# Optimization experiments

Hardware: AMD Instinct MI355X
Metric: run time of the kernel (lower is better)

The kernel has to match this reference:

```python
import jax, jax.numpy as jnp
import numpy as np

N_NODES = 100000
N_EDGES = 1600000
C = 256            # in_channels == out_channels
NUM_BUNDLES = 64
BUNDLE_DIM = 2
NUM_GRAPHS = 128
BN_EPS = 1e-5


def setup_inputs() -> dict:
    key = jax.random.key(0)
    ks = jax.random.split(key, 12)
    x = jax.random.normal(ks[0], (N_NODES, C), dtype=jnp.float32)
    edge_index = jax.random.randint(ks[1], (2, N_EDGES), 0, N_NODES, dtype=jnp.int64)
    batch = jnp.sort(jax.random.randint(ks[2], (N_NODES,), 0, NUM_GRAPHS, dtype=jnp.int64))
    s = 0.05
    # struct_enc MLP: Linear(C, 2*NB) -> GELU -> Linear(2*NB, NB)
    se_w1 = jax.random.normal(ks[3], (C, 2 * NUM_BUNDLES), dtype=jnp.float32) * s
    se_b1 = jnp.zeros((2 * NUM_BUNDLES,), dtype=jnp.float32)
    se_w2 = jax.random.normal(ks[4], (2 * NUM_BUNDLES, NUM_BUNDLES), dtype=jnp.float32) * s
    se_b2 = jnp.zeros((NUM_BUNDLES,), dtype=jnp.float32)
    # LimConv.lin: Linear(C, C)
    lin_w = jax.random.normal(ks[5], (C, C), dtype=jnp.float32) * s
    lin_b = jnp.zeros((C,), dtype=jnp.float32)
    # BatchNorm1d affine params
    bn_gamma = jnp.ones((C,), dtype=jnp.float32)
    bn_beta = jnp.zeros((C,), dtype=jnp.float32)
    return {"x": x, "edge_index": edge_index, "batch": batch,
            "se_w1": se_w1, "se_b1": se_b1, "se_w2": se_w2, "se_b2": se_b2,
            "lin_w": lin_w, "lin_b": lin_b, "bn_gamma": bn_gamma, "bn_beta": bn_beta}


def _lim_layer(x, batch, se_w1, se_b1, se_w2, se_b2, lin_w, lin_b, bn_gamma, bn_beta):
    n = x.shape[0]
    # vector field: [N, NB, 2, fiber]
    vf = x.reshape(n, NUM_BUNDLES, BUNDLE_DIM, -1)
    # struct_enc MLP -> per-bundle angle (tanh-squashed), euler map to SO(2)
    h1 = jax.nn.gelu(x @ se_w1 + se_b1, approximate=False)
    ang = jnp.tanh(h1 @ se_w2 + se_b2)          # [N, NB]
    c, s = jnp.cos(ang), jnp.sin(ang)
    # R[n,b] = [[c,-s],[s,c]]  -> [N, NB, 2, 2]
    rot = jnp.stack([jnp.stack([c, -s], axis=-1),
                     jnp.stack([s, c], axis=-1)], axis=-2)
    # rotate fibers
    vf = jnp.einsum('nbij,nbjf->nbif', rot, vf)
    h = vf.reshape(n, C) @ lin_w + lin_b
    # global mean pool over graphs, then broadcast back to nodes
    sums = jax.ops.segment_sum(h, batch, num_segments=NUM_GRAPHS)
    cnts = jax.ops.segment_sum(jnp.ones((n,), h.dtype), batch, num_segments=NUM_GRAPHS)
    hmean = sums / jnp.maximum(cnts, 1.0)[:, None]
    h = hmean[batch]
    # inverse rotation (R^T)
    vf = h.reshape(n, NUM_BUNDLES, BUNDLE_DIM, -1)
    vf = jnp.einsum('nbji,nbjf->nbif', rot, vf)
    h = vf.reshape(n, C)
    # residual (dim_in == dim_out)
    h = x + h
    # dropout p=0 / eval -> identity. BatchNorm1d with batch statistics.
    mu = jnp.mean(h, axis=0)
    var = jnp.var(h, axis=0)
    h = (h - mu) * jax.lax.rsqrt(var + BN_EPS) * bn_gamma + bn_beta
    return h


def reference(x, edge_index, batch, se_w1, se_b1, se_w2, se_b2, lin_w, lin_b, bn_gamma, bn_beta):
    # edge_index is unused when num_gnn == 0 (struct_enc is an MLP), as in the source.
    del edge_index
    return _lim_layer(x, batch, se_w1, se_b1, se_w2, se_b2, lin_w, lin_b, bn_gamma, bn_beta)
```

## Files before the change

### kernel.cpp

```cpp
#include <hip/hip_runtime.h>
#include <hip/hip_bf16.h>
#include <math.h>

#define N_NODES 100000
#define C 256
#define NB 64
#define H1D 128
#define NG 128
#define GS 257
#define BN_EPS 1e-5f

#define BLKN 64
#define NBLK1 ((N_NODES + BLKN - 1) / BLKN)

#define OFF_GSUMS 0
#define OFF_BNSUM (NG * GS)
#define OFF_BNSQ  (OFF_BNSUM + 256)
#define ZERO_FLOATS (OFF_BNSQ + 256)
#define OFF_HMEAN ZERO_FLOATS
#define OFF_WT1   (OFF_HMEAN + NG * C)
#define OFF_WT2   (OFF_WT1 + 16896)
#define OFF_CSN   (OFF_WT2 + 4352)

#define WT1_LD 264
#define WT2_LD 136
#define XS_LD  272

typedef __attribute__((ext_vector_type(8))) short bf16x8;
typedef __attribute__((ext_vector_type(4))) float f32x4;

struct __align__(8) bf4 { __hip_bfloat16 x, y, z, w; };

__device__ __forceinline__ float bf2f(__hip_bfloat16 h) { return __bfloat162float(h); }

__global__ __launch_bounds__(256)
void k0_prep(const float* __restrict__ W1, const float* __restrict__ W2,
             __hip_bfloat16* __restrict__ Wt1, __hip_bfloat16* __restrict__ Wt2)
{
    const int t0 = threadIdx.x + blockIdx.x * 256;
    const int stride = gridDim.x * 256;
    for (int i = t0; i < 128 * 256; i += stride) {
        int n = i >> 8, k = i & 255;
        Wt1[n * WT1_LD + k] = __float2bfloat16(W1[k * 128 + n]);
    }
    for (int i = t0; i < 64 * 128; i += stride) {
        int n = i >> 7, k = i & 127;
        Wt2[n * WT2_LD + k] = __float2bfloat16(W2[k * 64 + n]);
    }
}

__global__ __launch_bounds__(256, 3)
void k1_angles_rot_pool(const float* __restrict__ x,
                        const int* __restrict__ batch,
                        const __hip_bfloat16* __restrict__ Wt1g,
                        const float* __restrict__ b1,
                        const __hip_bfloat16* __restrict__ Wt2g,
                        const float* __restrict__ b2,
                        float* __restrict__ gsums,
                        __hip_bfloat16* __restrict__ csng)
{
    __shared__ __hip_bfloat16 xs[BLKN][XS_LD];
    __shared__ char sm_u[BLKN * WT2_LD * 2];
    __shared__ int gsh[BLKN];
    auto h1s = (__hip_bfloat16 (*)[WT2_LD])sm_u;
    auto csn = (__hip_bfloat16 (*)[132])sm_u;

    const int t = threadIdx.x;
    const int w = t >> 6;
    const int l = t & 63;
    const int lo = l & 15, quad = l >> 4;
    const int n0 = blockIdx.x * BLKN;
    const int nrem = min(BLKN, N_NODES - n0);

    #pragma unroll
    for (int m = 0; m < 16; ++m) {
        int idx = t + m * 256;
        int r = idx >> 6, c4 = (idx & 63) * 4;
        float4 v;
        if (n0 + r < N_NODES) v = *(const float4*)(x + (size_t)(n0 + r) * C + c4);
        else { v.x = v.y = v.z = v.w = 0.f; }
        bf4 pk;
        pk.x = __float2bfloat16(v.x); pk.y = __float2bfloat16(v.y);
        pk.z = __float2bfloat16(v.z); pk.w = __float2bfloat16(v.w);
        *(bf4*)&xs[r][c4] = pk;
    }
    if (t < BLKN) gsh[t] = batch[min(n0 + t, N_NODES - 1)];
    __syncthreads();

    const short* w1base = (const short*)Wt1g + (w * 32 + lo) * WT1_LD + quad * 8;
    f32x4 acc1[4][2];
    #pragma unroll
    for (int mt = 0; mt < 4; ++mt) { acc1[mt][0] = (f32x4)0.f; acc1[mt][1] = (f32x4)0.f; }
    #pragma unroll
    for (int k = 0; k < 8; ++k) {
        bf16x8 bA = *(const bf16x8*)(w1base + k * 32);
        bf16x8 bB = *(const bf16x8*)(w1base + 16 * WT1_LD + k * 32);
        #pragma unroll
        for (int mt = 0; mt < 4; ++mt) {
            bf16x8 afr = *(const bf16x8*)&xs[mt * 16 + lo][k * 32 + quad * 8];
            acc1[mt][0] = __builtin_amdgcn_mfma_f32_16x16x32_bf16(afr, bA, acc1[mt][0], 0, 0, 0);
            acc1[mt][1] = __builtin_amdgcn_mfma_f32_16x16x32_bf16(afr, bB, acc1[mt][1], 0, 0, 0);
        }
    }
    #pragma unroll
    for (int nt = 0; nt < 2; ++nt) {
        const float bb = b1[w * 32 + nt * 16 + lo];
        #pragma unroll
        for (int mt = 0; mt < 4; ++mt) {
            #pragma unroll
            for (int r = 0; r < 4; ++r) {
                float v = acc1[mt][nt][r] + bb;
                v = 0.5f * v * (1.0f + erff(v * 0.70710678118654752f));
                h1s[mt * 16 + quad * 4 + r][w * 32 + nt * 16 + lo] = __float2bfloat16(v);
            }
        }
    }
    __syncthreads();

    const short* w2base = (const short*)Wt2g + lo * WT2_LD + quad * 8;
    f32x4 acc2[4];
    #pragma unroll
    for (int nt = 0; nt < 4; ++nt) acc2[nt] = (f32x4)0.f;
    #pragma unroll
    for (int k = 0; k < 4; ++k) {
        bf16x8 afr = *(const bf16x8*)&h1s[w * 16 + lo][k * 32 + quad * 8];
        #pragma unroll
        for (int nt = 0; nt < 4; ++nt) {
            bf16x8 bfrg = *(const bf16x8*)(w2base + nt * 16 * WT2_LD + k * 32);
            acc2[nt] = __builtin_amdgcn_mfma_f32_16x16x32_bf16(afr, bfrg, acc2[nt], 0, 0, 0);
        }
    }
    __syncthreads();

    #pragma unroll
    for (int nt = 0; nt < 4; ++nt) {
        const float bb = b2[nt * 16 + lo];
        #pragma unroll
        for (int r = 0; r < 4; ++r) {
            float a = tanhf(acc2[nt][r] + bb);
            float sv, cv;
            sincosf(a, &sv, &cv);
            union { unsigned int u; __hip_bfloat16 h[2]; } p;
            p.h[0] = __float2bfloat16(cv);
            p.h[1] = __float2bfloat16(sv);
            *(unsigned int*)&csn[w * 16 + quad * 4 + r][2 * (nt * 16 + lo)] = p.u;
        }
    }
    __syncthreads();

    #pragma unroll
    for (int m = 0; m < 8; ++m) {
        int idx = t + m * 256;
        int row = idx >> 5;
        int d2 = (idx & 31);
        if (n0 + row < N_NODES) {
            uint2 v = *(const uint2*)&csn[row][d2 * 4];
            *(uint2*)(csng + (size_t)(n0 + row) * 128 + d2 * 4) = v;
        }
    }

    {
        const int b = t >> 2;
        const int idx2 = t & 3;
        const int i2 = idx2 >> 1;
        const int f = idx2 & 1;
        float racc = 0.f, rcnt = 0.f;
        int gprev = gsh[0];
        #pragma unroll 8
        for (int r = 0; r < BLKN; ++r) {
            const int g = gsh[r];
            if (g != gprev) {
                atomicAdd(&gsums[gprev * GS + t], racc);
                if (t == 0) atomicAdd(&gsums[gprev * GS + 256], rcnt);
                racc = 0.f; rcnt = 0.f; gprev = g;
            }
            bf4 xq = *(const bf4*)&xs[r][4 * b];
            union { unsigned int u; __hip_bfloat16 h[2]; } cs;
            cs.u = *(const unsigned int*)&csn[r][2 * b];
            const float x0 = f ? bf2f(xq.y) : bf2f(xq.x);
            const float x1 = f ? bf2f(xq.w) : bf2f(xq.z);
            const float cb = bf2f(cs.h[0]);
            const float sb = bf2f(cs.h[1]);
            racc += (i2 == 0) ? (cb * x0 - sb * x1) : (sb * x0 + cb * x1);
            rcnt += (r < nrem) ? 1.f : 0.f;
        }
        atomicAdd(&gsums[gprev * GS + t], racc);
        if (t == 0) atomicAdd(&gsums[gprev * GS + 256], rcnt);
    }
}

__global__ __launch_bounds__(256)
void k2_hmean(const float* __restrict__ gsums, const float* __restrict__ lin_w,
              const float* __restrict__ lin_b, float* __restrict__ hmean)
{
    __shared__ float gs[C];
    __shared__ float cnt_sh;
    const int g = blockIdx.x;
    const int t = threadIdx.x;
    gs[t] = gsums[g * GS + t];
    if (t == 0) cnt_sh = gsums[g * GS + 256];
    __syncthreads();
    float a0 = 0.f, a1 = 0.f, a2 = 0.f, a3 = 0.f;
    #pragma unroll 4
    for (int k = 0; k < C; k += 4) {
        a0 += gs[k + 0] * lin_w[(size_t)(k + 0) * C + t];
        a1 += gs[k + 1] * lin_w[(size_t)(k + 1) * C + t];
        a2 += gs[k + 2] * lin_w[(size_t)(k + 2) * C + t];
        a3 += gs[k + 3] * lin_w[(size_t)(k + 3) * C + t];
    }
    const float cnt = cnt_sh;
    hmean[g * C + t] = (cnt > 0.f) ? ((a0 + a1 + a2 + a3) / cnt + lin_b[t]) : 0.f;
}

__global__ __launch_bounds__(256, 4)
void k3_stats(const float* __restrict__ x,
              const int* __restrict__ batch,
              const __hip_bfloat16* __restrict__ csng,
              const float* __restrict__ hmean,
              float* __restrict__ bnsum, float* __restrict__ bnsq)
{
    __shared__ float rs[4][C];
    __shared__ float rq[4][C];
    const int t = threadIdx.x;
    const int s = t >> 6;
    const int cg = t & 63;
    float bs0 = 0.f, bs1 = 0.f, bs2 = 0.f, bs3 = 0.f;
    float bq0 = 0.f, bq1 = 0.f, bq2 = 0.f, bq3 = 0.f;

    for (int base = blockIdx.x * 4; base < N_NODES; base += gridDim.x * 4) {
        const int n = base + s;
        if (n < N_NODES) {
            const int g = batch[n];
            const float4 hm = *(const float4*)(hmean + (size_t)g * C + cg * 4);
            union { unsigned int u; __hip_bfloat16 h[2]; } cs;
            cs.u = *(const unsigned int*)(csng + (size_t)n * 128 + cg * 2);
            const float cv = bf2f(cs.h[0]);
            const float sv = bf2f(cs.h[1]);
            const float4 xv = *(const float4*)(x + (size_t)n * C + cg * 4);
            float4 o;
            o.x = xv.x + cv * hm.x + sv * hm.z;
            o.y = xv.y + cv * hm.y + sv * hm.w;
            o.z = xv.z - sv * hm.x + cv * hm.z;
            o.w = xv.w - sv * hm.y + cv * hm.w;
            bs0 += o.x; bs1 += o.y; bs2 += o.z; bs3 += o.w;
            bq0 += o.x * o.x; bq1 += o.y * o.y; bq2 += o.z * o.z; bq3 += o.w * o.w;
        }
    }
    rs[s][cg * 4 + 0] = bs0; rs[s][cg * 4 + 1] = bs1;
    rs[s][cg * 4 + 2] = bs2; rs[s][cg * 4 + 3] = bs3;
    rq[s][cg * 4 + 0] = bq0; rq[s][cg * 4 + 1] = bq1;
    rq[s][cg * 4 + 2] = bq2; rq[s][cg * 4 + 3] = bq3;
    __syncthreads();
    atomicAdd(&bnsum[t], rs[0][t] + rs[1][t] + rs[2][t] + rs[3][t]);
    atomicAdd(&bnsq[t],  rq[0][t] + rq[1][t] + rq[2][t] + rq[3][t]);
}

__global__ __launch_bounds__(256, 4)
void k4_fused(const float* __restrict__ x,
              const int* __restrict__ batch,
              const __hip_bfloat16* __restrict__ csng,
              const float* __restrict__ hmean,
              const float* __restrict__ bnsum, const float* __restrict__ bnsq,
              const float* __restrict__ gamma, const float* __restrict__ beta,
              float* __restrict__ out)
{
    __shared__ float mul_s[C], add_s[C];
    const int t = threadIdx.x;
    {
        const float inv_n = 1.0f / (float)N_NODES;
        const float mu = bnsum[t] * inv_n;
        const float var = bnsq[t] * inv_n - mu * mu;
        const float inv = rsqrtf(var + BN_EPS);
        const float m = gamma[t] * inv;
        mul_s[t] = m;
        add_s[t] = beta[t] - mu * m;
    }
    __syncthreads();
    const int s = t >> 6;
    const int cg = t & 63;
    const float4 mm = *(const float4*)&mul_s[cg * 4];
    const float4 aa = *(const float4*)&add_s[cg * 4];

    for (int base = blockIdx.x * 4; base < N_NODES; base += gridDim.x * 4) {
        const int n = base + s;
        if (n < N_NODES) {
            const int g = batch[n];
            const float4 hm = *(const float4*)(hmean + (size_t)g * C + cg * 4);
            union { unsigned int u; __hip_bfloat16 h[2]; } cs;
            cs.u = *(const unsigned int*)(csng + (size_t)n * 128 + cg * 2);
            const float cv = bf2f(cs.h[0]);
            const float sv = bf2f(cs.h[1]);
            const float4 xv = *(const float4*)(x + (size_t)n * C + cg * 4);
            float4 o;
            o.x = (xv.x + cv * hm.x + sv * hm.z) * mm.x + aa.x;
            o.y = (xv.y + cv * hm.y + sv * hm.w) * mm.y + aa.y;
            o.z = (xv.z - sv * hm.x + cv * hm.z) * mm.z + aa.z;
            o.w = (xv.w - sv * hm.y + cv * hm.w) * mm.w + aa.w;
            *(float4*)(out + (size_t)n * C + cg * 4) = o;
        }
    }
}

extern "C" void kernel_launch(void* const* d_in, const int* in_sizes, int n_in,
                              void* d_out, int out_size, void* d_ws, size_t ws_size,
                              hipStream_t stream)
{
    const float* x      = (const float*)d_in[0];
    const int* batch    = (const int*)d_in[2];
    const float* W1     = (const float*)d_in[3];
    const float* b1     = (const float*)d_in[4];
    const float* W2     = (const float*)d_in[5];
    const float* b2     = (const float*)d_in[6];
    const float* lin_w  = (const float*)d_in[7];
    const float* lin_b  = (const float*)d_in[8];
    const float* gamma  = (const float*)d_in[9];
    const float* beta   = (const float*)d_in[10];

    float* ws    = (float*)d_ws;
    float* gsums = ws + OFF_GSUMS;
    float* bnsum = ws + OFF_BNSUM;
    float* bnsq  = ws + OFF_BNSQ;
    float* hmean = ws + OFF_HMEAN;
    __hip_bfloat16* Wt1  = (__hip_bfloat16*)(ws + OFF_WT1);
    __hip_bfloat16* Wt2  = (__hip_bfloat16*)(ws + OFF_WT2);
    __hip_bfloat16* csng = (__hip_bfloat16*)(ws + OFF_CSN);
    float* out   = (float*)d_out;

    hipMemsetAsync(gsums, 0, ZERO_FLOATS * sizeof(float), stream);

    k0_prep<<<32, 256, 0, stream>>>(W1, W2, Wt1, Wt2);
    k1_angles_rot_pool<<<NBLK1, 256, 0, stream>>>(x, batch, Wt1, b1, Wt2, b2,
                                                  gsums, csng);
    k2_hmean<<<NG, 256, 0, stream>>>(gsums, lin_w, lin_b, hmean);
    k3_stats<<<1024, 256, 0, stream>>>(x, batch, csng, hmean, bnsum, bnsq);
    k4_fused<<<2048, 256, 0, stream>>>(x, batch, csng, hmean, bnsum, bnsq,
                                       gamma, beta, out);
}
```

Measured before the change: 346.9 us.

## Fold BatchNorm statistics into pooling pass via per-graph moment sums

Removes the separate k3 statistics pass, which re-read x and csn for every node. k1 now also accumulates per-graph moments (x·cos, x·sin, cos, sin, cos², cos·sin) plus per-channel x sums and squares. k2 then derives the BatchNorm sum and sum-of-squares in closed form from these moments and hmean. It also halves the node tile to 32 rows with higher occupancy, and swaps erf-GELU, tanh and sincos for fast approximations (tanh-form GELU, __expf, __sinf/__cosf), at some cost in numerical accuracy. It also drops the bounds checks, relying on N_NODES being divisible by 32, and the expanded squares risk cancellation error in the variance.

```diff
diff --git a/kernel.cpp b/kernel.cpp
--- a/kernel.cpp
+++ b/kernel.cpp
@@ -7,14 +7,15 @@
 #define NB 64
 #define H1D 128
 #define NG 128
-#define GS 257
 #define BN_EPS 1e-5f
 
-#define BLKN 64
-#define NBLK1 ((N_NODES + BLKN - 1) / BLKN)
+#define BLKN 32
+#define NBLK1 (N_NODES / BLKN)
+
+#define GREC 769
 
 #define OFF_GSUMS 0
-#define OFF_BNSUM (NG * GS)
+#define OFF_BNSUM (NG * GREC)
 #define OFF_BNSQ  (OFF_BNSUM + 256)
 #define ZERO_FLOATS (OFF_BNSQ + 256)
 #define OFF_HMEAN ZERO_FLOATS
@@ -33,6 +34,15 @@
 
 __device__ __forceinline__ float bf2f(__hip_bfloat16 h) { return __bfloat162float(h); }
 
+__device__ __forceinline__ float fast_tanh(float y) {
+    float e = __expf(2.f * y);
+    return 1.f - 2.f / (e + 1.f);
+}
+__device__ __forceinline__ float fast_gelu(float v) {
+    float u = 0.7978845608f * (v + 0.044715f * v * v * v);
+    return 0.5f * v * (1.f + fast_tanh(u));
+}
+
 __global__ __launch_bounds__(256)
 void k0_prep(const float* __restrict__ W1, const float* __restrict__ W2,
              __hip_bfloat16* __restrict__ Wt1, __hip_bfloat16* __restrict__ Wt2)
@@ -49,7 +59,7 @@
     }
 }
 
-__global__ __launch_bounds__(256, 3)
+__global__ __launch_bounds__(256, 6)
 void k1_angles_rot_pool(const float* __restrict__ x,
                         const int* __restrict__ batch,
                         const __hip_bfloat16* __restrict__ Wt1g,
@@ -57,6 +67,7 @@
                         const __hip_bfloat16* __restrict__ Wt2g,
                         const float* __restrict__ b2,
                         float* __restrict__ gsums,
+                        float* __restrict__ bnsum, float* __restrict__ bnsq,
                         __hip_bfloat16* __restrict__ csng)
 {
     __shared__ __hip_bfloat16 xs[BLKN][XS_LD];
@@ -70,33 +81,30 @@
     const int l = t & 63;
     const int lo = l & 15, quad = l >> 4;
     const int n0 = blockIdx.x * BLKN;
-    const int nrem = min(BLKN, N_NODES - n0);
-
-    #pragma unroll
-    for (int m = 0; m < 16; ++m) {
+
+    #pragma unroll
+    for (int m = 0; m < 8; ++m) {
         int idx = t + m * 256;
         int r = idx >> 6, c4 = (idx & 63) * 4;
-        float4 v;
-        if (n0 + r < N_NODES) v = *(const float4*)(x + (size_t)(n0 + r) * C + c4);
-        else { v.x = v.y = v.z = v.w = 0.f; }
+        float4 v = *(const float4*)(x + (size_t)(n0 + r) * C + c4);
         bf4 pk;
         pk.x = __float2bfloat16(v.x); pk.y = __float2bfloat16(v.y);
         pk.z = __float2bfloat16(v.z); pk.w = __float2bfloat16(v.w);
         *(bf4*)&xs[r][c4] = pk;
     }
-    if (t < BLKN) gsh[t] = batch[min(n0 + t, N_NODES - 1)];
+    if (t < BLKN) gsh[t] = batch[n0 + t];
     __syncthreads();
 
     const short* w1base = (const short*)Wt1g + (w * 32 + lo) * WT1_LD + quad * 8;
-    f32x4 acc1[4][2];
-    #pragma unroll
-    for (int mt = 0; mt < 4; ++mt) { acc1[mt][0] = (f32x4)0.f; acc1[mt][1] = (f32x4)0.f; }
+    f32x4 acc1[2][2];
+    #pragma unroll
+    for (int mt = 0; mt < 2; ++mt) { acc1[mt][0] = (f32x4)0.f; acc1[mt][1] = (f32x4)0.f; }
     #pragma unroll
     for (int k = 0; k < 8; ++k) {
         bf16x8 bA = *(const bf16x8*)(w1base + k * 32);
         bf16x8 bB = *(const bf16x8*)(w1base + 16 * WT1_LD + k * 32);
         #pragma unroll
-        for (int mt = 0; mt < 4; ++mt) {
+        for (int mt = 0; mt < 2; ++mt) {
             bf16x8 afr = *(const bf16x8*)&xs[mt * 16 + lo][k * 32 + quad * 8];
             acc1[mt][0] = __builtin_amdgcn_mfma_f32_16x16x32_bf16(afr, bA, acc1[mt][0], 0, 0, 0);
             acc1[mt][1] = __builtin_amdgcn_mfma_f32_16x16x32_bf16(afr, bB, acc1[mt][1], 0, 0, 0);
@@ -106,153 +114,149 @@
     for (int nt = 0; nt < 2; ++nt) {
         const float bb = b1[w * 32 + nt * 16 + lo];
         #pragma unroll
-        for (int mt = 0; mt < 4; ++mt) {
+        for (int mt = 0; mt < 2; ++mt) {
             #pragma unroll
             for (int r = 0; r < 4; ++r) {
-                float v = acc1[mt][nt][r] + bb;
-                v = 0.5f * v * (1.0f + erff(v * 0.70710678118654752f));
+                float v = fast_gelu(acc1[mt][nt][r] + bb);
                 h1s[mt * 16 + quad * 4 + r][w * 32 + nt * 16 + lo] = __float2bfloat16(v);
             }
         }
     }
     __syncthreads();
 
-    const short* w2base = (const short*)Wt2g + lo * WT2_LD + quad * 8;
-    f32x4 acc2[4];
-    #pragma unroll
-    for (int nt = 0; nt < 4; ++nt) acc2[nt] = (f32x4)0.f;
+    const int mw = w >> 1;
+    const int nb0 = (w & 1) * 32;
+    const short* w2base = (const short*)Wt2g + (nb0 + lo) * WT2_LD + quad * 8;
+    f32x4 acc2[2];
+    acc2[0] = (f32x4)0.f; acc2[1] = (f32x4)0.f;
     #pragma unroll
     for (int k = 0; k < 4; ++k) {
-        bf16x8 afr = *(const bf16x8*)&h1s[w * 16 + lo][k * 32 + quad * 8];
-        #pragma unroll
-        for (int nt = 0; nt < 4; ++nt) {
-            bf16x8 bfrg = *(const bf16x8*)(w2base + nt * 16 * WT2_LD + k * 32);
-            acc2[nt] = __builtin_amdgcn_mfma_f32_16x16x32_bf16(afr, bfrg, acc2[nt], 0, 0, 0);
-        }
-    }
-    __syncthreads();
-
-    #pragma unroll
-    for (int nt = 0; nt < 4; ++nt) {
-        const float bb = b2[nt * 16 + lo];
+        bf16x8 afr = *(const bf16x8*)&h1s[mw * 16 + lo][k * 32 + quad * 8];
+        bf16x8 bA = *(const bf16x8*)(w2base + k * 32);
+        bf16x8 bB = *(const bf16x8*)(w2base + 16 * WT2_LD + k * 32);
+        acc2[0] = __builtin_amdgcn_mfma_f32_16x16x32_bf16(afr, bA, acc2[0], 0, 0, 0);
+        acc2[1] = __builtin_amdgcn_mfma_f32_16x16x32_bf16(afr, bB, acc2[1], 0, 0, 0);
+    }
+    __syncthreads();
+
+    #pragma unroll
+    for (int nt = 0; nt < 2; ++nt) {
+        const int col = nb0 + nt * 16 + lo;
+        const float bb = b2[col];
         #pragma unroll
         for (int r = 0; r < 4; ++r) {
-            float a = tanhf(acc2[nt][r] + bb);
-            float sv, cv;
-            sincosf(a, &sv, &cv);
+            float a = fast_tanh(acc2[nt][r] + bb);
             union { unsigned int u; __hip_bfloat16 h[2]; } p;
-            p.h[0] = __float2bfloat16(cv);
-            p.h[1] = __float2bfloat16(sv);
-            *(unsigned int*)&csn[w * 16 + quad * 4 + r][2 * (nt * 16 + lo)] = p.u;
-        }
-    }
-    __syncthreads();
-
-    #pragma unroll
-    for (int m = 0; m < 8; ++m) {
+            p.h[0] = __float2bfloat16(__cosf(a));
+            p.h[1] = __float2bfloat16(__sinf(a));
+            *(unsigned int*)&csn[mw * 16 + quad * 4 + r][2 * col] = p.u;
+        }
+    }
+    __syncthreads();
+
+    #pragma unroll
+    for (int m = 0; m < 4; ++m) {
         int idx = t + m * 256;
         int row = idx >> 5;
-        int d2 = (idx & 31);
-        if (n0 + row < N_NODES) {
-            uint2 v = *(const uint2*)&csn[row][d2 * 4];
-            *(uint2*)(csng + (size_t)(n0 + row) * 128 + d2 * 4) = v;
-        }
+        int q = (idx & 31);
+        uint2 v = *(const uint2*)&csn[row][q * 4];
+        *(uint2*)(csng + (size_t)(n0 + row) * 128 + q * 4) = v;
     }
 
     {
-        const int b = t >> 2;
-        const int idx2 = t & 3;
-        const int i2 = idx2 >> 1;
-        const int f = idx2 & 1;
-        float racc = 0.f, rcnt = 0.f;
+        const int c = t;
+        const int b = c >> 2;
+        const int idx2 = c & 3;
+        float xc_a = 0.f, xs_a = 0.f, xm = 0.f, xq = 0.f, st = 0.f, rcnt = 0.f;
         int gprev = gsh[0];
         #pragma unroll 8
         for (int r = 0; r < BLKN; ++r) {
             const int g = gsh[r];
             if (g != gprev) {
-                atomicAdd(&gsums[gprev * GS + t], racc);
-                if (t == 0) atomicAdd(&gsums[gprev * GS + 256], rcnt);
-                racc = 0.f; rcnt = 0.f; gprev = g;
+                float* rec = gsums + (size_t)gprev * GREC;
+                atomicAdd(&rec[c], xc_a);
+                atomicAdd(&rec[256 + c], xs_a);
+                atomicAdd(&rec[512 + t], st);
+                if (t == 0) atomicAdd(&rec[768], rcnt);
+                xc_a = 0.f; xs_a = 0.f; st = 0.f; rcnt = 0.f; gprev = g;
             }
-            bf4 xq = *(const bf4*)&xs[r][4 * b];
+            const float xv = bf2f(xs[r][c]);
             union { unsigned int u; __hip_bfloat16 h[2]; } cs;
             cs.u = *(const unsigned int*)&csn[r][2 * b];
-            const float x0 = f ? bf2f(xq.y) : bf2f(xq.x);
-            const float x1 = f ? bf2f(xq.w) : bf2f(xq.z);
-            const float cb = bf2f(cs.h[0]);
-            const float sb = bf2f(cs.h[1]);
-            racc += (i2 == 0) ? (cb * x0 - sb * x1) : (sb * x0 + cb * x1);
-            rcnt += (r < nrem) ? 1.f : 0.f;
-        }
-        atomicAdd(&gsums[gprev * GS + t], racc);
-        if (t == 0) atomicAdd(&gsums[gprev * GS + 256], rcnt);
+            const float cv = bf2f(cs.h[0]);
+            const float sv = bf2f(cs.h[1]);
+            xc_a += xv * cv;
+            xs_a += xv * sv;
+            xm += xv;
+            xq += xv * xv;
+            st += (idx2 == 0) ? cv : (idx2 == 1) ? sv : (idx2 == 2) ? cv * cv : cv * sv;
+            rcnt += 1.f;
+        }
+        float* rec = gsums + (size_t)gprev * GREC;
+        atomicAdd(&rec[c], xc_a);
+        atomicAdd(&rec[256 + c], xs_a);
+        atomicAdd(&rec[512 + t], st);
+        if (t == 0) atomicAdd(&rec[768], rcnt);
+        atomicAdd(&bnsum[c], xm);
+        atomicAdd(&bnsq[c], xq);
     }
 }
 
 __global__ __launch_bounds__(256)
-void k2_hmean(const float* __restrict__ gsums, const float* __restrict__ lin_w,
-              const float* __restrict__ lin_b, float* __restrict__ hmean)
-{
-    __shared__ float gs[C];
+void k2_hmean_stats(const float* __restrict__ gsums,
+                    const float* __restrict__ lin_w, const float* __restrict__ lin_b,
+                    float* __restrict__ hmean,
+                    float* __restrict__ bnsum, float* __restrict__ bnsq)
+{
+    __shared__ float xc[C], xsv[C], bs4[C], grot[C], hm[C];
     __shared__ float cnt_sh;
     const int g = blockIdx.x;
     const int t = threadIdx.x;
-    gs[t] = gsums[g * GS + t];
-    if (t == 0) cnt_sh = gsums[g * GS + 256];
-    __syncthreads();
+    const float* rec = gsums + (size_t)g * GREC;
+    xc[t]  = rec[t];
+    xsv[t] = rec[256 + t];
+    bs4[t] = rec[512 + t];
+    if (t == 0) cnt_sh = rec[768];
+    __syncthreads();
+
+    const int b = t >> 2, idx2 = t & 3, i2 = idx2 >> 1;
+    grot[t] = (i2 == 0) ? (xc[t] - xsv[t + 2]) : (xsv[t - 2] + xc[t]);
+    __syncthreads();
+
     float a0 = 0.f, a1 = 0.f, a2 = 0.f, a3 = 0.f;
     #pragma unroll 4
     for (int k = 0; k < C; k += 4) {
-        a0 += gs[k + 0] * lin_w[(size_t)(k + 0) * C + t];
-        a1 += gs[k + 1] * lin_w[(size_t)(k + 1) * C + t];
-        a2 += gs[k + 2] * lin_w[(size_t)(k + 2) * C + t];
-        a3 += gs[k + 3] * lin_w[(size_t)(k + 3) * C + t];
+        a0 += grot[k + 0] * lin_w[(size_t)(k + 0) * C + t];
+        a1 += grot[k + 1] * lin_w[(size_t)(k + 1) * C + t];
+        a2 += grot[k + 2] * lin_w[(size_t)(k + 2) * C + t];
+        a3 += grot[k + 3] * lin_w[(size_t)(k + 3) * C + t];
     }
     const float cnt = cnt_sh;
-    hmean[g * C + t] = (cnt > 0.f) ? ((a0 + a1 + a2 + a3) / cnt + lin_b[t]) : 0.f;
-}
-
-__global__ __launch_bounds__(256, 4)
-void k3_stats(const float* __restrict__ x,
-              const int* __restrict__ batch,
-              const __hip_bfloat16* __restrict__ csng,
-              const float* __restrict__ hmean,
-              float* __restrict__ bnsum, float* __restrict__ bnsq)
-{
-    __shared__ float rs[4][C];
-    __shared__ float rq[4][C];
-    const int t = threadIdx.x;
-    const int s = t >> 6;
-    const int cg = t & 63;
-    float bs0 = 0.f, bs1 = 0.f, bs2 = 0.f, bs3 = 0.f;
-    float bq0 = 0.f, bq1 = 0.f, bq2 = 0.f, bq3 = 0.f;
-
-    for (int base = blockIdx.x * 4; base < N_NODES; base += gridDim.x * 4) {
-        const int n = base + s;
-        if (n < N_NODES) {
-            const int g = batch[n];
-            const float4 hm = *(const float4*)(hmean + (size_t)g * C + cg * 4);
-            union { unsigned int u; __hip_bfloat16 h[2]; } cs;
-            cs.u = *(const unsigned int*)(csng + (size_t)n * 128 + cg * 2);
-            const float cv = bf2f(cs.h[0]);
-            const float sv = bf2f(cs.h[1]);
-            const float4 xv = *(const float4*)(x + (size_t)n * C + cg * 4);
-            float4 o;
-            o.x = xv.x + cv * hm.x + sv * hm.z;
-            o.y = xv.y + cv * hm.y + sv * hm.w;
-            o.z = xv.z - sv * hm.x + cv * hm.z;
-            o.w = xv.w - sv * hm.y + cv * hm.w;
-            bs0 += o.x; bs1 += o.y; bs2 += o.z; bs3 += o.w;
-            bq0 += o.x * o.x; bq1 += o.y * o.y; bq2 += o.z * o.z; bq3 += o.w * o.w;
-        }
-    }
-    rs[s][cg * 4 + 0] = bs0; rs[s][cg * 4 + 1] = bs1;
-    rs[s][cg * 4 + 2] = bs2; rs[s][cg * 4 + 3] = bs3;
-    rq[s][cg * 4 + 0] = bq0; rq[s][cg * 4 + 1] = bq1;
-    rq[s][cg * 4 + 2] = bq2; rq[s][cg * 4 + 3] = bq3;
-    __syncthreads();
-    atomicAdd(&bnsum[t], rs[0][t] + rs[1][t] + rs[2][t] + rs[3][t]);
-    atomicAdd(&bnsq[t],  rq[0][t] + rq[1][t] + rq[2][t] + rq[3][t]);
+    const float hv = (cnt > 0.f) ? ((a0 + a1 + a2 + a3) / cnt + lin_b[t]) : 0.f;
+    hm[t] = hv;
+    hmean[g * C + t] = hv;
+    __syncthreads();
+
+    if (cnt > 0.f) {
+        const int f = idx2 & 1;
+        const float h0 = hm[4 * b + f];
+        const float h1 = hm[4 * b + 2 + f];
+        const float CV = bs4[4 * b + 0], SV = bs4[4 * b + 1];
+        const float CC = bs4[4 * b + 2], CS = bs4[4 * b + 3];
+        const float SS = cnt - CC;
+        float sumc, sqc;
+        if (i2 == 0) {
+            sumc = h0 * CV + h1 * SV;
+            sqc  = 2.f * (h0 * xc[t] + h1 * xsv[t])
+                 + h0 * h0 * CC + 2.f * h0 * h1 * CS + h1 * h1 * SS;
+        } else {
+            sumc = -h0 * SV + h1 * CV;
+            sqc  = 2.f * (-h0 * xsv[t] + h1 * xc[t])
+                 + h0 * h0 * SS - 2.f * h0 * h1 * CS + h1 * h1 * CC;
+        }
+        atomicAdd(&bnsum[t], sumc);
+        atomicAdd(&bnsq[t], sqc);
+    }
 }
 
 __global__ __launch_bounds__(256, 4)
@@ -330,9 +334,8 @@
 
     k0_prep<<<32, 256, 0, stream>>>(W1, W2, Wt1, Wt2);
     k1_angles_rot_pool<<<NBLK1, 256, 0, stream>>>(x, batch, Wt1, b1, Wt2, b2,
-                                                  gsums, csng);
-    k2_hmean<<<NG, 256, 0, stream>>>(gsums, lin_w, lin_b, hmean);
-    k3_stats<<<1024, 256, 0, stream>>>(x, batch, csng, hmean, bnsum, bnsq);
+                                                  gsums, bnsum, bnsq, csng);
+    k2_hmean_stats<<<NG, 256, 0, stream>>>(gsums, lin_w, lin_b, hmean, bnsum, bnsq);
     k4_fused<<<2048, 256, 0, stream>>>(x, batch, csng, hmean, bnsum, bnsq,
                                        gamma, beta, out);
 }
```

Result: faster. 319.1 us (-8.0%).
